# Performance work log

Measured on AMD Instinct MI355X. Metric: run time of the kernel, lower is better.

The kernel has to match this reference:

```python
import jax, jax.numpy as jnp
import numpy as np
from jax import lax

REGION_SIZE = 5      # local window side (init kwarg)
BANDWIDTH = 0.1      # KDE kernel bandwidth (init kwarg)
NUM_BINS = 256       # intensity histogram bins
EPS = 1e-10


def setup_inputs() -> dict:
    key = jax.random.key(0)
    # image-like inputs in [0, 255] to match the 256 intensity bins
    x = jax.random.uniform(key, (8, 3, 96, 96), dtype=jnp.float32) * 255.0
    return {"x": x}


def reference(x):
    # x: [B, C, H, W]
    bins = jnp.arange(NUM_BINS, dtype=x.dtype)            # [256]
    # derivative-of-sigmoid KDE kernel evaluated at each (pixel, bin) pair
    d = (x[..., None] - bins) / BANDWIDTH                 # [B,C,H,W,256]
    sig = jax.nn.sigmoid(d)
    k = sig * (1.0 - sig)                                 # [B,C,H,W,256]
    # accumulate kernel mass over the region_size x region_size window
    # (stride 1, centered -> SAME padding), per bin
    p = lax.reduce_window(
        k, jnp.float32(0.0), lax.add,
        window_dimensions=(1, 1, REGION_SIZE, REGION_SIZE, 1),
        window_strides=(1, 1, 1, 1, 1),
        padding='SAME')                                   # [B,C,H,W,256]
    # normalize to a probability distribution over bins
    p = p / (jnp.sum(p, axis=-1, keepdims=True) + EPS)
    # Shannon entropy per pixel
    return -jnp.sum(p * jnp.log(p + EPS), axis=-1)        # [B,C,H,W]
```

## Files before the change

kernel.cpp:

```cpp
#include <hip/hip_runtime.h>
#include <hip/hip_fp16.h>
#include <stdint.h>


#define W 96
#define H 96
#define TPB 256

__global__ __launch_bounds__(TPB) void entropy_kde_kernel(
    const float* __restrict__ x, float* __restrict__ out, int total)
{
    const int pid = blockIdx.x * TPB + threadIdx.x;
    if (pid >= total) return;

    const int xcol = pid % W;
    const int y    = (pid / W) % H;
    const int img  = pid / (W * H);
    const float* __restrict__ base = x + img * (H * W);

    float va[25];
    #pragma unroll
    for (int i = 0; i < 25; ++i) {
        const int dy = i / 5 - 2, dx = i % 5 - 2;
        const int yy = y + dy,    xx = xcol + dx;
        va[i] = base[min(max(yy, 0), H - 1) * W + min(max(xx, 0), W - 1)];
    }

    int      b0a[25];
    uint32_t pk [25];
    float S = 0.f;
    #pragma unroll
    for (int i = 0; i < 25; ++i) {
        const int dy = i / 5 - 2, dx = i % 5 - 2;
        const int yy = y + dy,    xx = xcol + dx;
        const bool ok = (yy >= 0) & (yy < H) & (xx >= 0) & (xx < W);
        const float v  = va[i];
        const int   b0 = (int)v;
        const float f  = v - (float)b0;
        const float E  = __expf(-10.f * f);
        const float E2 = __expf(10.f * f - 10.f);
        const float r0 = __builtin_amdgcn_rcpf(1.f + E);
        const float r1 = __builtin_amdgcn_rcpf(1.f + E2);
        const float k0 = ok ? E  * r0 * r0 : 0.f;
        const float k1 = ok ? E2 * r1 * r1 : 0.f;
        const __half2 hk = __floats2half2_rn(k0, k1);
        const float2  kc = __half22float2(hk);
        S += kc.x + kc.y;
        b0a[i] = b0;
        pk[i]  = __builtin_bit_cast(uint32_t, hk);
    }

    float T0 = 0.f, T1 = 0.f, T2 = 0.f, T3 = 0.f;
    #pragma unroll
    for (int i = 0; i < 25; ++i) {
        const int b0i = b0a[i];
        uint32_t Ppk = 0u;
        #pragma unroll
        for (int j = 0; j < i; ++j) {
            const int d = b0i - b0a[j];
            const uint32_t pj = pk[j];
            uint32_t t = (d == 0)  ? pj         : 0u;
            t          = (d == 1)  ? (pj >> 16) : t;
            t          = (d == -1) ? (pj << 16) : t;
            const __half2 sum = __hadd2(__builtin_bit_cast(__half2, Ppk),
                                        __builtin_bit_cast(__half2, t));
            Ppk = __builtin_bit_cast(uint32_t, sum);
        }
        const float2 P  = __half22float2(__builtin_bit_cast(__half2, Ppk));
        const float2 kc = __half22float2(__builtin_bit_cast(__half2, pk[i]));
        const float z0 = P.x + kc.x, z1 = P.y + kc.y;
        const float t4 = z0  * __logf(z0  + 1e-10f) - P.x * __logf(P.x + 1e-10f)
                       + z1  * __logf(z1  + 1e-10f) - P.y * __logf(P.y + 1e-10f);
        if      ((i & 3) == 0) T0 += t4;
        else if ((i & 3) == 1) T1 += t4;
        else if ((i & 3) == 2) T2 += t4;
        else                   T3 += t4;
    }
    const float T  = (T0 + T1) + (T2 + T3);
    const float Sp = S + 1e-10f;
    out[pid] = __logf(Sp) - T / Sp;
}

extern "C" void kernel_launch(void* const* d_in, const int* in_sizes, int n_in,
                              void* d_out, int out_size, void* d_ws, size_t ws_size,
                              hipStream_t stream)
{
    const float* x = (const float*)d_in[0];
    float* out = (float*)d_out;
    const int total  = in_sizes[0];
    const int blocks = (total + TPB - 1) / TPB;
    entropy_kde_kernel<<<blocks, TPB, 0, stream>>>(x, out, total);
}
```

Measured before the change: 85.56 us.

## Split per-pixel window work across two wavefronts and combine via shared memory

Each pixel's 25-sample triangular pairwise loop is now split between two wavefronts. One handles samples 0..17 and the other 18..24, with the split chosen to roughly balance the O(i) inner work. Their partial S and T sums are combined through shared memory after a barrier. This doubles the thread count to raise parallelism and occupancy, and the launch-bounds hint asks for 6 blocks. The three-way select in the inner loop is also replaced by a clamped 64-bit shift, and the number of accumulators drops. In exchange the wavefronts recompute overlapping kernel values, the kernel pays for a barrier and shared-memory traffic, and the grid assumes the total is divisible by 128.

After: 120.2 us. 40.5% more time.

```diff
diff --git a/kernel.cpp b/kernel.cpp
--- a/kernel.cpp
+++ b/kernel.cpp
@@ -6,31 +6,25 @@
 #define W 96
 #define H 96
 #define TPB 256
+#define SPLIT 18
 
-__global__ __launch_bounds__(TPB) void entropy_kde_kernel(
-    const float* __restrict__ x, float* __restrict__ out, int total)
+template<int NB, int I0>
+__device__ __forceinline__ void role_compute(const float* __restrict__ base,
+                                             int xcol, int y,
+                                             float& Sout, float& Tout)
 {
-    const int pid = blockIdx.x * TPB + threadIdx.x;
-    if (pid >= total) return;
-
-    const int xcol = pid % W;
-    const int y    = (pid / W) % H;
-    const int img  = pid / (W * H);
-    const float* __restrict__ base = x + img * (H * W);
-
-    float va[25];
+    float va[NB];
     #pragma unroll
-    for (int i = 0; i < 25; ++i) {
+    for (int i = 0; i < NB; ++i) {
         const int dy = i / 5 - 2, dx = i % 5 - 2;
         const int yy = y + dy,    xx = xcol + dx;
         va[i] = base[min(max(yy, 0), H - 1) * W + min(max(xx, 0), W - 1)];
     }
 
-    int      b0a[25];
-    uint32_t pk [25];
+    int b0a[NB]; uint32_t pk[NB];
     float S = 0.f;
     #pragma unroll
-    for (int i = 0; i < 25; ++i) {
+    for (int i = 0; i < NB; ++i) {
         const int dy = i / 5 - 2, dx = i % 5 - 2;
         const int yy = y + dy,    xx = xcol + dx;
         const bool ok = (yy >= 0) & (yy < H) & (xx >= 0) & (xx < W);
@@ -44,24 +38,25 @@
         const float k0 = ok ? E  * r0 * r0 : 0.f;
         const float k1 = ok ? E2 * r1 * r1 : 0.f;
         const __half2 hk = __floats2half2_rn(k0, k1);
-        const float2  kc = __half22float2(hk);
-        S += kc.x + kc.y;
+        if (i >= I0) {
+            const float2 kc = __half22float2(hk);
+            S += kc.x + kc.y;
+        }
         b0a[i] = b0;
         pk[i]  = __builtin_bit_cast(uint32_t, hk);
     }
 
-    float T0 = 0.f, T1 = 0.f, T2 = 0.f, T3 = 0.f;
+    float T0 = 0.f, T1 = 0.f;
     #pragma unroll
-    for (int i = 0; i < 25; ++i) {
+    for (int i = I0; i < NB; ++i) {
         const int b0i = b0a[i];
         uint32_t Ppk = 0u;
         #pragma unroll
         for (int j = 0; j < i; ++j) {
             const int d = b0i - b0a[j];
-            const uint32_t pj = pk[j];
-            uint32_t t = (d == 0)  ? pj         : 0u;
-            t          = (d == 1)  ? (pj >> 16) : t;
-            t          = (d == -1) ? (pj << 16) : t;
+            int s = 16 * d + 32;
+            s = s < 0 ? 0 : (s > 63 ? 63 : s);
+            const uint32_t t = (uint32_t)((((uint64_t)pk[j]) << 32) >> s);
             const __half2 sum = __hadd2(__builtin_bit_cast(__half2, Ppk),
                                         __builtin_bit_cast(__half2, t));
             Ppk = __builtin_bit_cast(uint32_t, sum);
@@ -69,16 +64,43 @@
         const float2 P  = __half22float2(__builtin_bit_cast(__half2, Ppk));
         const float2 kc = __half22float2(__builtin_bit_cast(__half2, pk[i]));
         const float z0 = P.x + kc.x, z1 = P.y + kc.y;
-        const float t4 = z0  * __logf(z0  + 1e-10f) - P.x * __logf(P.x + 1e-10f)
-                       + z1  * __logf(z1  + 1e-10f) - P.y * __logf(P.y + 1e-10f);
-        if      ((i & 3) == 0) T0 += t4;
-        else if ((i & 3) == 1) T1 += t4;
-        else if ((i & 3) == 2) T2 += t4;
-        else                   T3 += t4;
+        const float t4 = z0 * __logf(z0 + 1e-10f) - P.x * __logf(P.x + 1e-10f)
+                       + z1 * __logf(z1 + 1e-10f) - P.y * __logf(P.y + 1e-10f);
+        if (i & 1) T1 += t4; else T0 += t4;
     }
-    const float T  = (T0 + T1) + (T2 + T3);
-    const float Sp = S + 1e-10f;
-    out[pid] = __logf(Sp) - T / Sp;
+    Sout = S;
+    Tout = T0 + T1;
+}
+
+__global__ __launch_bounds__(TPB, 6) void entropy_kde_kernel(
+    const float* __restrict__ x, float* __restrict__ out, int total)
+{
+    __shared__ float sS[128], sT[128];
+    const int tid  = threadIdx.x;
+    const int wv   = tid >> 6;
+    const int g    = wv >> 1;
+    const int r    = wv & 1;
+    const int l    = tid & 63;
+    const int slot = g * 64 + l;
+    const int px   = blockIdx.x * 128 + slot;
+
+    const int xcol = px % W;
+    const int y    = (px / W) % H;
+    const int img  = px / (W * H);
+    const float* __restrict__ base = x + img * (H * W);
+
+    float S, T;
+    if (r == 0) role_compute<SPLIT, 0>(base, xcol, y, S, T);
+    else        role_compute<25, SPLIT>(base, xcol, y, S, T);
+
+    if (r == 1) { sS[slot] = S; sT[slot] = T; }
+    __syncthreads();
+    if (r == 0) {
+        S += sS[slot];
+        T += sT[slot];
+        const float Sp = S + 1e-10f;
+        if (px < total) out[px] = __logf(Sp) - T / Sp;
+    }
 }
 
 extern "C" void kernel_launch(void* const* d_in, const int* in_sizes, int n_in,
@@ -88,6 +110,6 @@
     const float* x = (const float*)d_in[0];
     float* out = (float*)d_out;
     const int total  = in_sizes[0];
-    const int blocks = (total + TPB - 1) / TPB;
+    const int blocks = total / 128;
     entropy_kde_kernel<<<blocks, TPB, 0, stream>>>(x, out, total);
 }
```
